# Performance work log

Hardware: AMD Instinct MI355X
Metric: run time of the kernel (lower is better)

Reference implementation:

```python
import jax, jax.numpy as jnp
import numpy as np

C, L, B = 66, 100, 4096
FEAT = 9 * C * 12  # 7128


def _conv1d(x, w, b, pad):
    # x: (B, Cin, L), w: (Cout, Cin, K), b: (Cout,)
    y = jax.lax.conv_general_dilated(x, w, (1,), [(pad, pad)],
                                     dimension_numbers=('NCH', 'OIH', 'NCH'))
    return y + b[None, :, None]


def _pool2(x):
    # AvgPool1d(kernel=2, stride=2) with floor on odd lengths
    Lx = x.shape[-1]
    x = x[..., : 2 * (Lx // 2)]
    return x.reshape(*x.shape[:-1], Lx // 2, 2).mean(-1)


def _branch(xc, w1, b1, w2, b2, w3, b3, pad):
    # conv/relu/pool x3 (dropout is identity in eval)
    h = _pool2(jax.nn.relu(_conv1d(xc, w1, b1, pad)))
    h = _pool2(jax.nn.relu(_conv1d(h, w2, b2, pad)))
    h = _pool2(jax.nn.relu(_conv1d(h, w3, b3, pad)))
    return h  # (B, 4, 12)


def setup_inputs() -> dict:
    key = jax.random.key(0)
    ks = jax.random.split(key, 20)
    s = 0.1
    inp = {
        'x': jax.random.normal(ks[0], (B, L, C), dtype=jnp.float32),
        # high-resolution branch (kernel 7, pad 3), one filter set per channel
        'hw1': jax.random.normal(ks[1], (C, 8, 1, 7)) * s,
        'hb1': jnp.full((C, 8), 0.1, jnp.float32),
        'hw2': jax.random.normal(ks[2], (C, 4, 8, 7)) * s,
        'hb2': jnp.full((C, 4), 0.1, jnp.float32),
        'hw3': jax.random.normal(ks[3], (C, 4, 4, 7)) * s,
        'hb3': jnp.full((C, 4), 0.1, jnp.float32),
        # low-resolution branch (kernel 3, pad 1)
        'lw1': jax.random.normal(ks[4], (C, 8, 1, 3)) * s,
        'lb1': jnp.full((C, 8), 0.1, jnp.float32),
        'lw2': jax.random.normal(ks[5], (C, 4, 8, 3)) * s,
        'lb2': jnp.full((C, 4), 0.1, jnp.float32),
        'lw3': jax.random.normal(ks[6], (C, 4, 4, 3)) * s,
        'lb3': jnp.full((C, 4), 0.1, jnp.float32),
        # MLP head
        'fw1': jax.random.normal(ks[7], (1936, FEAT)) * 0.02,
        'fb1': jnp.full((1936,), 0.1, jnp.float32),
        'fw2': jax.random.normal(ks[8], (14, 1936)) * 0.02,
        'fb2': jnp.full((14,), 0.1, jnp.float32),
    }
    return inp


def reference(x, hw1, hb1, hw2, hb2, hw3, hb3,
              lw1, lb1, lw2, lb2, lw3, lb3, fw1, fb1, fw2, fb2):
    bsz = x.shape[0]
    xc = jnp.transpose(x, (2, 0, 1))[:, :, None, :]  # (C, B, 1, L)
    high = jax.vmap(lambda xi, a, b_, c, d, e, f: _branch(xi, a, b_, c, d, e, f, 3))(
        xc, hw1, hb1, hw2, hb2, hw3, hb3)        # (C, B, 4, 12)
    low = jax.vmap(lambda xi, a, b_, c, d, e, f: _branch(xi, a, b_, c, d, e, f, 1))(
        xc, lw1, lb1, lw2, lb2, lw3, lb3)        # (C, B, 4, 12)
    res = jax.vmap(lambda xi: _pool2(_pool2(_pool2(xi))))(xc)  # (C, B, 1, 12)
    feats = jnp.concatenate([high, low, res], axis=2)          # (C, B, 9, 12)
    feats = jnp.transpose(feats, (1, 0, 2, 3)).reshape(bsz, -1)  # (B, C*9*12)
    h = jax.nn.relu(feats @ fw1.T + fb1)
    return h @ fw2.T + fb2
```

## Files before the change

kernel.cpp:

```cpp
#include <hip/hip_runtime.h>

typedef _Float16 f16;
typedef _Float16 h2 __attribute__((ext_vector_type(2)));
typedef _Float16 f16x8 __attribute__((ext_vector_type(8)));
typedef float    f32x4 __attribute__((ext_vector_type(4)));
typedef unsigned int u32;
typedef u32 u32x2 __attribute__((ext_vector_type(2)));
typedef u32 u32x4 __attribute__((ext_vector_type(4)));

#define CCH 66
#define LLEN 100
#define BSZ 4096
#define NPAD 2048
#define NOUT 1936
#define KFEAT 7128
#define FPC 112
#define KF2 (CCH * FPC)
#define KP2 7424
#define NCH2 (KP2 / 8)
#define ROWE (BSZ * 8)
#define LC (LLEN * CCH)
#define OSTR 25
#define XPW 52
#define CWS 512

typedef __attribute__((address_space(1))) const u32 gu32;
typedef __attribute__((address_space(3))) u32 lu32;

__device__ __forceinline__ void gload_lds16(const void* g, void* l) {
    __builtin_amdgcn_global_load_lds((gu32*)g, (lu32*)l, 16, 0, 0);
}

__device__ __forceinline__ h2  uh(u32 v) { return __builtin_bit_cast(h2, v); }
__device__ __forceinline__ u32 hu(h2 v)  { return __builtin_bit_cast(u32, v); }
__device__ __forceinline__ h2  pkfma(h2 a, h2 b, h2 c) { return __builtin_elementwise_fma(a, b, c); }
__device__ __forceinline__ h2  pkmax0(h2 a) { h2 z = (h2)(_Float16)0.f; return __builtin_elementwise_max(a, z); }

__global__ __launch_bounds__(256) void xpose_pack(const float* __restrict__ x,
                                                  u32* __restrict__ xP) {
    __shared__ float tile[64][133];
    const int w = blockIdx.x;
    const int b0 = blockIdx.y * 64;
    const int tid = threadIdx.x;
    const float* src = x + (size_t)b0 * LC + (size_t)(2 * w) * CCH;
#pragma unroll
    for (int i = 0; i < 33; ++i) {
        int f = i * 256 + tid;
        int bi = f / 132, j = f - bi * 132;
        tile[bi][j] = src[(size_t)bi * LC + j];
    }
    __syncthreads();
    const int lane = tid & 63, cg = tid >> 6;
    for (int c = cg; c < CCH; c += 4) {
        u32 v = hu((h2){(_Float16)tile[lane][c], (_Float16)tile[lane][66 + c]});
        xP[((size_t)c * XPW + w) * BSZ + b0 + lane] = v;
    }
}

__global__ __launch_bounds__(256) void zero_halo_xp(u32* __restrict__ xP) {
    const int c = blockIdx.x;
    const int i = blockIdx.y * 256 + threadIdx.x;
    *(u32x4*)(xP + ((size_t)c * XPW + 50) * BSZ + (size_t)i * 4) = (u32x4){0u, 0u, 0u, 0u};
}

__device__ __forceinline__ u32 dupf(float v) {
    _Float16 h = (_Float16)v; return hu((h2){h, h});
}
__device__ __forceinline__ u32 pk2f(float a, float b) {
    return hu((h2){(_Float16)a, (_Float16)b});
}

__global__ __launch_bounds__(64) void prep_w(
    const float* __restrict__ hw1, const float* __restrict__ hb1,
    const float* __restrict__ hw2, const float* __restrict__ hb2,
    const float* __restrict__ hw3, const float* __restrict__ hb3,
    const float* __restrict__ lw1, const float* __restrict__ lb1,
    const float* __restrict__ lw2, const float* __restrict__ lb2,
    const float* __restrict__ lw3, const float* __restrict__ lb3,
    u32* __restrict__ wpk) {
    const int c = blockIdx.x, t = threadIdx.x;
    u32* wb = wpk + c * CWS;
    for (int i = t; i < 56; i += 64) wb[i] = dupf(hw1[c * 56 + i]);
    if (t < 8)  wb[56 + t] = dupf(hb1[c * 8 + t]);
    for (int i = t; i < 224; i += 64) wb[64 + i] = dupf(hw2[c * 224 + i]);
    if (t < 4)  wb[288 + t] = dupf(hb2[c * 4 + t]);
    for (int i = t; i < 56; i += 64) {
        int pr = i / 28, j = i - pr * 28;
        wb[292 + i] = pk2f(hw3[c * 112 + 2 * pr * 28 + j], hw3[c * 112 + (2 * pr + 1) * 28 + j]);
    }
    if (t < 2)  wb[348 + t] = pk2f(hb3[c * 4 + 2 * t], hb3[c * 4 + 2 * t + 1]);
    for (int i = t; i < 24; i += 64) wb[350 + i] = dupf(lw1[c * 24 + i]);
    if (t < 8)  wb[374 + t] = dupf(lb1[c * 8 + t]);
    for (int i = t; i < 96; i += 64) wb[382 + i] = dupf(lw2[c * 96 + i]);
    if (t < 4)  wb[478 + t] = dupf(lb2[c * 4 + t]);
    for (int i = t; i < 24; i += 64) {
        int pr = i / 12, j = i - pr * 12;
        wb[482 + i] = pk2f(lw3[c * 48 + 2 * pr * 12 + j], lw3[c * 48 + (2 * pr + 1) * 12 + j]);
    }
    if (t < 2)  wb[506 + t] = pk2f(lb3[c * 4 + 2 * t], lb3[c * 4 + 2 * t + 1]);
}

template<int K>
__device__ __forceinline__ void hp1_core(const u32* PX, const u32* __restrict__ w1d,
                                         const u32* __restrict__ b1d, u32 msk, u32 np[8]) {
#pragma unroll
    for (int ic = 0; ic < 8; ++ic) {
        h2 bb = uh(b1d[ic]);
        h2 AL = bb, AH = bb;
#pragma unroll
        for (int k = 0; k < K; ++k) {
            h2 w = uh(w1d[ic * K + k]);
            AL = pkfma(w, uh(PX[k]), AL);
            AH = pkfma(w, uh(PX[k + 2]), AH);
        }
        AL = pkmax0(AL); AH = pkmax0(AH);
        _Float16 cA = (_Float16)0.5f * (AL.x + AL.y);
        _Float16 cB = (_Float16)0.5f * (AH.x + AH.y);
        np[ic] = hu((h2){cA, cB}) & msk;
    }
}

template<int K, int NA>
__device__ __forceinline__ void hp1_win(const u32 A[NA], int idx,
                                        const u32* w1d, const u32* b1d, u32 np[8]) {
    u32 PX[K + 2];
#pragma unroll
    for (int j = 0; j < K + 2; ++j)
        PX[j] = (j & 1) ? A[(j + 1) / 2]
                        : __builtin_amdgcn_alignbit(A[j / 2 + 1], A[j / 2], 16);
    u32 m = ((idx < 50) ? 0xFFFFu : 0u) | ((idx + 1 < 50) ? 0xFFFF0000u : 0u);
    hp1_core<K>(PX, w1d, b1d, m, np);
}

template<int K, int IDX>
__device__ __forceinline__ void hp1_edge(const u32* __restrict__ xg,
                                         const u32* w1d, const u32* b1d, u32 np[8]) {
    constexpr int P = K / 2;
    u32 PX[K + 2];
#pragma unroll
    for (int j = 0; j < K + 2; ++j) {
        int u = 2 * IDX - P + j;
        u32 v;
        if (u < -1)      v = 0u;
        else if (u == -1) v = xg[0] << 16;
        else if (u & 1)  v = __builtin_amdgcn_alignbit(xg[(size_t)((u + 1) / 2) * BSZ],
                                                       xg[(size_t)((u - 1) / 2) * BSZ], 16);
        else             v = xg[(size_t)(u / 2) * BSZ];
        PX[j] = v;
    }
    hp1_core<K>(PX, w1d, b1d, 0xFFFFFFFFu, np);
}

template<int K>
__device__ __forceinline__ void run_branch_pk(const u32* __restrict__ xg,
                                              const u32* __restrict__ wb,
                                              u32* __restrict__ orow) {
    constexpr int P = K / 2;
    constexpr int NW1 = (K + 1) / 2;
    constexpr int NA = (K == 7) ? 6 : 4;
    constexpr int WB = (K == 7) ? 3 : 2;
    const u32* w1d = wb;
    const u32* b1d = wb + 8 * K;
    const u32* w2d = b1d + 8;
    const u32* b2d = w2d + 32 * K;
    const u32* w3p = b2d + 4;
    const u32* b3p = w3p + 8 * K;

    u32 W1p[8][NW1];
    u32 W2d[4][K];
#pragma unroll
    for (int ic = 0; ic < 8; ++ic)
#pragma unroll
        for (int j = 0; j < NW1; ++j) W1p[ic][j] = 0u;
#pragma unroll
    for (int oc = 0; oc < 4; ++oc)
#pragma unroll
        for (int k = 0; k < K; ++k) W2d[oc][k] = 0u;

    {
        u32 np[8];
        if (K == 7) {
            hp1_edge<K, 0>(xg, w1d, b1d, np);
#pragma unroll
            for (int ic = 0; ic < 8; ++ic) W1p[ic][1] = np[ic] << 16;
            hp1_edge<K, 1>(xg, w1d, b1d, np);
#pragma unroll
            for (int ic = 0; ic < 8; ++ic) W1p[ic][2] = np[ic];
            hp1_edge<K, 3>(xg, w1d, b1d, np);
#pragma unroll
            for (int ic = 0; ic < 8; ++ic) W1p[ic][3] = np[ic];
        } else {
            hp1_edge<K, 0>(xg, w1d, b1d, np);
#pragma unroll
            for (int ic = 0; ic < 8; ++ic) W1p[ic][0] = np[ic] << 16;
            hp1_edge<K, 1>(xg, w1d, b1d, np);
#pragma unroll
            for (int ic = 0; ic < 8; ++ic) W1p[ic][1] = np[ic];
        }
    }

    u32 XA[NA];
#pragma unroll
    for (int j = 0; j < NA; ++j) XA[j] = xg[(size_t)(WB + j) * BSZ];

    h2 Pp01 = (h2)(_Float16)0.f, Pp23 = Pp01, Q01 = Pp01, Q23 = Pp01;
    const int SMAX = 23 + P;
    for (int s = 0; s <= SMAX; ++s) {
        h2 Y[4];
#pragma unroll
        for (int oc = 0; oc < 4; ++oc) Y[oc] = uh(b2d[oc]);
#pragma unroll
        for (int ic = 0; ic < 8; ++ic) {
            u32 PW[K];
#pragma unroll
            for (int k = 0; k < K; ++k)
                PW[k] = (k & 1) ? __builtin_amdgcn_alignbit(W1p[ic][k / 2 + 1], W1p[ic][k / 2], 16)
                                : W1p[ic][k / 2];
#pragma unroll
            for (int oc = 0; oc < 4; ++oc)
#pragma unroll
                for (int k = 0; k < K; ++k)
                    Y[oc] = pkfma(uh(w2d[(oc * 8 + ic) * K + k]), uh(PW[k]), Y[oc]);
        }
#pragma unroll
        for (int oc = 0; oc < 4; ++oc) {
            h2 Yr = pkmax0(Y[oc]);
            _Float16 hv = (_Float16)0.5f * (Yr.x + Yr.y);
            u32 d = hu((h2){hv, hv});
            d = (s <= 24) ? d : 0u;
#pragma unroll
            for (int k = 0; k < K - 1; ++k) W2d[oc][k] = W2d[oc][k + 1];
            W2d[oc][K - 1] = d;
        }
        int p = s - P;
        if (p >= 0) {
            h2 Y01 = uh(b3p[0]), Y23 = uh(b3p[1]);
#pragma unroll
            for (int ic = 0; ic < 4; ++ic)
#pragma unroll
                for (int k = 0; k < K; ++k) {
                    h2 wv = uh(W2d[ic][k]);
                    Y01 = pkfma(uh(w3p[ic * K + k]), wv, Y01);
                    Y23 = pkfma(uh(w3p[4 * K + ic * K + k]), wv, Y23);
                }
            Y01 = pkmax0(Y01); Y23 = pkmax0(Y23);
            if ((p & 1) == 0) { Pp01 = Y01; Pp23 = Y23; }
            else {
                h2 hf = (h2)(_Float16)0.5f;
                h2 O01 = (Pp01 + Y01) * hf;
                h2 O23 = (Pp23 + Y23) * hf;
                int t = p >> 1;
                if ((t & 1) == 0) { Q01 = O01; Q23 = O23; }
                else {
                    int w = t >> 1;
                    orow[0 * 6 + w] = hu((h2){Q01.x, O01.x});
                    orow[1 * 6 + w] = hu((h2){Q01.y, O01.y});
                    orow[2 * 6 + w] = hu((h2){Q23.x, O23.x});
                    orow[3 * 6 + w] = hu((h2){Q23.y, O23.y});
                }
            }
        }
        if (s < SMAX) {
            u32 np[8];
            hp1_win<K, NA>(XA, 2 * s + P + 2, w1d, b1d, np);
#pragma unroll
            for (int ic = 0; ic < 8; ++ic) {
#pragma unroll
                for (int j = 0; j < NW1 - 1; ++j) W1p[ic][j] = W1p[ic][j + 1];
                W1p[ic][NW1 - 1] = np[ic];
            }
#pragma unroll
            for (int j = 0; j < NA - 2; ++j) XA[j] = XA[j + 2];
            XA[NA - 2] = xg[(size_t)(WB + 2 * s + NA) * BSZ];
            XA[NA - 1] = xg[(size_t)(WB + 2 * s + NA + 1) * BSZ];
        }
    }
}

__global__ __launch_bounds__(256, 2) void feats_kernel(
    const u32* __restrict__ xP, const u32* __restrict__ wpk,
    f16* __restrict__ feats2) {
    __shared__ u32 obufw[256 * OSTR];
    const int c = blockIdx.x;
    const int tid = threadIdx.x;
    const int b = blockIdx.y * 256 + tid;

    const u32* xg = xP + (size_t)c * XPW * BSZ + b;
    const u32* wb = wpk + c * CWS;
    u32* orow = obufw + tid * OSTR;
    u32* dst = (u32*)feats2 + (size_t)c * 14 * (ROWE / 2) + (size_t)b * 4;

    run_branch_pk<7>(xg, wb, orow);
    {
        u32 v[24];
#pragma unroll
        for (int j = 0; j < 24; ++j) v[j] = orow[j];
#pragma unroll
        for (int ch = 0; ch < 6; ++ch)
            *(u32x4*)(dst + (size_t)ch * (ROWE / 2)) =
                (u32x4){v[ch * 4], v[ch * 4 + 1], v[ch * 4 + 2], v[ch * 4 + 3]};
    }
    run_branch_pk<3>(xg, wb + 350, orow);
    {
        u32 v[24];
#pragma unroll
        for (int j = 0; j < 24; ++j) v[j] = orow[j];
#pragma unroll
        for (int ch = 0; ch < 6; ++ch)
            *(u32x4*)(dst + (size_t)(6 + ch) * (ROWE / 2)) =
                (u32x4){v[ch * 4], v[ch * 4 + 1], v[ch * 4 + 2], v[ch * 4 + 3]};
    }
    u32 orr[6];
#pragma unroll
    for (int t2 = 0; t2 < 6; ++t2) {
        h2 S0 = uh(xg[(size_t)(8 * t2 + 0) * BSZ]) + uh(xg[(size_t)(8 * t2 + 1) * BSZ]) +
                uh(xg[(size_t)(8 * t2 + 2) * BSZ]) + uh(xg[(size_t)(8 * t2 + 3) * BSZ]);
        h2 S1 = uh(xg[(size_t)(8 * t2 + 4) * BSZ]) + uh(xg[(size_t)(8 * t2 + 5) * BSZ]) +
                uh(xg[(size_t)(8 * t2 + 6) * BSZ]) + uh(xg[(size_t)(8 * t2 + 7) * BSZ]);
        _Float16 o0 = (_Float16)0.125f * (S0.x + S0.y);
        _Float16 o1 = (_Float16)0.125f * (S1.x + S1.y);
        orr[t2] = hu((h2){o0, o1});
    }
    *(u32x4*)(dst + (size_t)12 * (ROWE / 2)) = (u32x4){orr[0], orr[1], orr[2], orr[3]};
    *(u32x4*)(dst + (size_t)13 * (ROWE / 2)) = (u32x4){orr[4], orr[5], 0u, 0u};
}

__global__ void zero_pad2(f16* __restrict__ feats2) {
    int idx = blockIdx.x * 256 + threadIdx.x;
    u32* dst = (u32*)(feats2 + (size_t)(CCH * 14) * ROWE);
    if (idx < (4 * ROWE * 2) / 16)
        *(u32x4*)(dst + idx * 4) = (u32x4){0u, 0u, 0u, 0u};
}

__global__ void cvt_fw1(const float* __restrict__ fw1, f16* __restrict__ dst) {
    int n = blockIdx.y;
    int kp = blockIdx.x * 256 + threadIdx.x;
    if (kp >= KP2) return;
    int c2 = kp / FPC, f = kp - c2 * FPC;
    float v = 0.f;
    if (n < NOUT && kp < KF2 && f < 108)
        v = fw1[(size_t)n * KFEAT + c2 * 108 + f];
    dst[(size_t)n * KP2 + kp] = (f16)v;
}

__global__ __launch_bounds__(256) void fc1_gemm(
    const f16* __restrict__ A, const f16* __restrict__ Bw, float* __restrict__ C) {
    __shared__ f16 lds_a[128 * 32];
    __shared__ f16 lds_b[128 * 32];
    const int tid = threadIdx.x;
    const int bm = blockIdx.x, bn = blockIdx.y, kz = blockIdx.z;
    const int wid = tid >> 6, lane = tid & 63;
    const int wm = wid >> 1, wn = wid & 1;

    f32x4 acc[4][4];
#pragma unroll
    for (int i = 0; i < 4; ++i)
#pragma unroll
        for (int j = 0; j < 4; ++j) acc[i][j] = (f32x4){0.f, 0.f, 0.f, 0.f};

    const f16* Bbase = Bw + (size_t)bn * 128 * KP2;
    const int l15 = lane & 15, lhi = lane >> 4;

    const int flat0 = tid, flat1 = 256 + tid;
    const int row0 = flat0 >> 2, kc0 = flat0 & 3;
    const int row1 = flat1 >> 2, kc1 = flat1 & 3;

    const int kbeg = kz * (KP2 / 2), kend = kbeg + KP2 / 2;
    for (int k0 = kbeg; k0 < kend; k0 += 32) {
        __syncthreads();
        gload_lds16(A + (size_t)((k0 >> 3) + kc0) * ROWE + (size_t)(bm * 128 + row0) * 8,
                    (char*)lds_a + flat0 * 16);
        gload_lds16(A + (size_t)((k0 >> 3) + kc1) * ROWE + (size_t)(bm * 128 + row1) * 8,
                    (char*)lds_a + flat1 * 16);
        gload_lds16(Bbase + (size_t)row0 * KP2 + k0 + kc0 * 8, (char*)lds_b + flat0 * 16);
        gload_lds16(Bbase + (size_t)row1 * KP2 + k0 + kc1 * 8, (char*)lds_b + flat1 * 16);
        __syncthreads();

        f16x8 af[4], bf[4];
#pragma unroll
        for (int i = 0; i < 4; ++i) {
            int m = wm * 64 + i * 16 + l15;
            af[i] = *(const f16x8*)(lds_a + m * 32 + lhi * 8);
            int n = wn * 64 + i * 16 + l15;
            bf[i] = *(const f16x8*)(lds_b + n * 32 + lhi * 8);
        }
#pragma unroll
        for (int i = 0; i < 4; ++i)
#pragma unroll
            for (int j = 0; j < 4; ++j)
                acc[i][j] = __builtin_amdgcn_mfma_f32_16x16x32_f16(af[i], bf[j], acc[i][j], 0, 0, 0);
    }

#pragma unroll
    for (int i = 0; i < 4; ++i)
#pragma unroll
        for (int j = 0; j < 4; ++j) {
            int n = bn * 128 + wn * 64 + j * 16 + l15;
#pragma unroll
            for (int r = 0; r < 4; ++r) {
                int m = bm * 128 + wm * 64 + i * 16 + lhi * 4 + r;
                atomicAdd(&C[(size_t)m * NPAD + n], acc[i][j][r]);
            }
        }
}

__global__ __launch_bounds__(256) void fc1_fin(const float* __restrict__ C,
                                               const float* __restrict__ fb1,
                                               f16* __restrict__ H) {
    size_t i4 = ((size_t)blockIdx.x * 256 + threadIdx.x) * 4;
    int n = (int)(i4 & (NPAD - 1));
    f32x4 v = *(const f32x4*)(C + i4);
    f16 r[4];
#pragma unroll
    for (int j = 0; j < 4; ++j) {
        int nn = n + j;
        float bias = (nn < NOUT) ? fb1[nn] : 0.f;
        r[j] = (f16)fmaxf(v[j] + bias, 0.f);
    }
    *(u32x2*)(H + i4) = (u32x2){hu((h2){r[0], r[1]}), hu((h2){r[2], r[3]})};
}

__global__ __launch_bounds__(64) void fc2_kernel(const f16* __restrict__ H,
                                                 const float* __restrict__ fw2,
                                                 const float* __restrict__ fb2,
                                                 float* __restrict__ out) {
    const int b = blockIdx.x;
    const int t = threadIdx.x;
    const f16* hb = H + (size_t)b * NPAD;
    float acc[14];
#pragma unroll
    for (int o = 0; o < 14; ++o) acc[o] = 0.f;
    for (int k = t; k < NOUT; k += 64) {
        float hv = (float)hb[k];
#pragma unroll
        for (int o = 0; o < 14; ++o) acc[o] += hv * fw2[o * NOUT + k];
    }
#pragma unroll
    for (int o = 0; o < 14; ++o) {
        float v = acc[o];
#pragma unroll
        for (int off = 32; off > 0; off >>= 1) v += __shfl_down(v, off, 64);
        if (t == 0) out[b * 14 + o] = v + fb2[o];
    }
}

extern "C" void kernel_launch(void* const* d_in, const int* in_sizes, int n_in,
                              void* d_out, int out_size, void* d_ws, size_t ws_size,
                              hipStream_t stream) {
    const float* x   = (const float*)d_in[0];
    const float* hw1 = (const float*)d_in[1];
    const float* hb1 = (const float*)d_in[2];
    const float* hw2 = (const float*)d_in[3];
    const float* hb2 = (const float*)d_in[4];
    const float* hw3 = (const float*)d_in[5];
    const float* hb3 = (const float*)d_in[6];
    const float* lw1 = (const float*)d_in[7];
    const float* lb1 = (const float*)d_in[8];
    const float* lw2 = (const float*)d_in[9];
    const float* lb2 = (const float*)d_in[10];
    const float* lw3 = (const float*)d_in[11];
    const float* lb3 = (const float*)d_in[12];
    const float* fw1 = (const float*)d_in[13];
    const float* fb1 = (const float*)d_in[14];
    const float* fw2 = (const float*)d_in[15];
    const float* fb2 = (const float*)d_in[16];

    char* wsb = (char*)d_ws;
    f16*  feats2 = (f16*)wsb;
    char* reg2   = wsb + (size_t)NCH2 * ROWE * 2;
    float* C     = (float*)reg2;
    f16*  h      = (f16*)(reg2 + (size_t)BSZ * NPAD * 4);
    char* reg3   = reg2 + 54067200;
    u32*  xP     = (u32*)reg3;
    f16*  fw1H   = (f16*)reg3;
    u32*  wpk    = (u32*)(reg3 + (size_t)CCH * XPW * BSZ * 4);

    xpose_pack<<<dim3(50, BSZ / 64), 256, 0, stream>>>(x, xP);
    zero_halo_xp<<<dim3(CCH, 8), 256, 0, stream>>>(xP);
    prep_w<<<dim3(CCH), 64, 0, stream>>>(hw1, hb1, hw2, hb2, hw3, hb3,
                                         lw1, lb1, lw2, lb2, lw3, lb3, wpk);
    feats_kernel<<<dim3(CCH, BSZ / 256), 256, 0, stream>>>(xP, wpk, feats2);
    zero_pad2<<<dim3(64), 256, 0, stream>>>(feats2);
    cvt_fw1<<<dim3((KP2 + 255) / 256, NPAD), 256, 0, stream>>>(fw1, fw1H);
    hipMemsetAsync(C, 0, (size_t)BSZ * NPAD * 4, stream);
    fc1_gemm<<<dim3(BSZ / 128, NPAD / 128, 2), 256, 0, stream>>>(feats2, fw1H, C);
    fc1_fin<<<dim3(BSZ * NPAD / 4 / 256), 256, 0, stream>>>(C, fb1, h);
    fc2_kernel<<<dim3(BSZ), 64, 0, stream>>>(h, fw2, fb2, (float*)d_out);
}
```

Measured before the change: 757.1 us.

## Drop split-K atomics in FC1 GEMM, fuse bias+ReLU epilogue, split feature branches

The FC1 GEMM no longer splits K across two blocks with fp32 atomicAdd into a zeroed buffer. Each block now runs the full K loop and writes the fp16 H output directly with bias and ReLU applied, which removes the memset, the atomics, the separate finalize kernel and a 32 MB fp32 intermediate. The feature kernel also gains a z dimension of 2, so the high- and low-resolution branches run in separate blocks for more parallelism. In exchange the GEMM grid is halved to 512 blocks, which may underfill the GPU, and the output stores are scalar fp16 writes.

After: 692.9 us. 1.09x faster.

```diff
diff --git a/kernel.cpp b/kernel.cpp
--- a/kernel.cpp
+++ b/kernel.cpp
@@ -290,8 +290,8 @@
     u32* orow = obufw + tid * OSTR;
     u32* dst = (u32*)feats2 + (size_t)c * 14 * (ROWE / 2) + (size_t)b * 4;
 
-    run_branch_pk<7>(xg, wb, orow);
-    {
+    if (blockIdx.z == 0) {
+        run_branch_pk<7>(xg, wb, orow);
         u32 v[24];
 #pragma unroll
         for (int j = 0; j < 24; ++j) v[j] = orow[j];
@@ -299,9 +299,8 @@
         for (int ch = 0; ch < 6; ++ch)
             *(u32x4*)(dst + (size_t)ch * (ROWE / 2)) =
                 (u32x4){v[ch * 4], v[ch * 4 + 1], v[ch * 4 + 2], v[ch * 4 + 3]};
-    }
-    run_branch_pk<3>(xg, wb + 350, orow);
-    {
+    } else {
+        run_branch_pk<3>(xg, wb + 350, orow);
         u32 v[24];
 #pragma unroll
         for (int j = 0; j < 24; ++j) v[j] = orow[j];
@@ -309,20 +308,20 @@
         for (int ch = 0; ch < 6; ++ch)
             *(u32x4*)(dst + (size_t)(6 + ch) * (ROWE / 2)) =
                 (u32x4){v[ch * 4], v[ch * 4 + 1], v[ch * 4 + 2], v[ch * 4 + 3]};
-    }
-    u32 orr[6];
-#pragma unroll
-    for (int t2 = 0; t2 < 6; ++t2) {
-        h2 S0 = uh(xg[(size_t)(8 * t2 + 0) * BSZ]) + uh(xg[(size_t)(8 * t2 + 1) * BSZ]) +
-                uh(xg[(size_t)(8 * t2 + 2) * BSZ]) + uh(xg[(size_t)(8 * t2 + 3) * BSZ]);
-        h2 S1 = uh(xg[(size_t)(8 * t2 + 4) * BSZ]) + uh(xg[(size_t)(8 * t2 + 5) * BSZ]) +
-                uh(xg[(size_t)(8 * t2 + 6) * BSZ]) + uh(xg[(size_t)(8 * t2 + 7) * BSZ]);
-        _Float16 o0 = (_Float16)0.125f * (S0.x + S0.y);
-        _Float16 o1 = (_Float16)0.125f * (S1.x + S1.y);
-        orr[t2] = hu((h2){o0, o1});
-    }
-    *(u32x4*)(dst + (size_t)12 * (ROWE / 2)) = (u32x4){orr[0], orr[1], orr[2], orr[3]};
-    *(u32x4*)(dst + (size_t)13 * (ROWE / 2)) = (u32x4){orr[4], orr[5], 0u, 0u};
+        u32 orr[6];
+#pragma unroll
+        for (int t2 = 0; t2 < 6; ++t2) {
+            h2 S0 = uh(xg[(size_t)(8 * t2 + 0) * BSZ]) + uh(xg[(size_t)(8 * t2 + 1) * BSZ]) +
+                    uh(xg[(size_t)(8 * t2 + 2) * BSZ]) + uh(xg[(size_t)(8 * t2 + 3) * BSZ]);
+            h2 S1 = uh(xg[(size_t)(8 * t2 + 4) * BSZ]) + uh(xg[(size_t)(8 * t2 + 5) * BSZ]) +
+                    uh(xg[(size_t)(8 * t2 + 6) * BSZ]) + uh(xg[(size_t)(8 * t2 + 7) * BSZ]);
+            _Float16 o0 = (_Float16)0.125f * (S0.x + S0.y);
+            _Float16 o1 = (_Float16)0.125f * (S1.x + S1.y);
+            orr[t2] = hu((h2){o0, o1});
+        }
+        *(u32x4*)(dst + (size_t)12 * (ROWE / 2)) = (u32x4){orr[0], orr[1], orr[2], orr[3]};
+        *(u32x4*)(dst + (size_t)13 * (ROWE / 2)) = (u32x4){orr[4], orr[5], 0u, 0u};
+    }
 }
 
 __global__ void zero_pad2(f16* __restrict__ feats2) {
@@ -344,11 +343,13 @@
 }
 
 __global__ __launch_bounds__(256) void fc1_gemm(
-    const f16* __restrict__ A, const f16* __restrict__ Bw, float* __restrict__ C) {
+    const f16* __restrict__ A, const f16* __restrict__ Bw,
+    const float* __restrict__ fb1, f16* __restrict__ H) {
     __shared__ f16 lds_a[128 * 32];
     __shared__ f16 lds_b[128 * 32];
     const int tid = threadIdx.x;
-    const int bm = blockIdx.x, bn = blockIdx.y, kz = blockIdx.z;
+    const int bm = blockIdx.x;
+    const int bn = blockIdx.y;
     const int wid = tid >> 6, lane = tid & 63;
     const int wm = wid >> 1, wn = wid & 1;
 
@@ -365,8 +366,7 @@
     const int row0 = flat0 >> 2, kc0 = flat0 & 3;
     const int row1 = flat1 >> 2, kc1 = flat1 & 3;
 
-    const int kbeg = kz * (KP2 / 2), kend = kbeg + KP2 / 2;
-    for (int k0 = kbeg; k0 < kend; k0 += 32) {
+    for (int k0 = 0; k0 < KP2; k0 += 32) {
         __syncthreads();
         gload_lds16(A + (size_t)((k0 >> 3) + kc0) * ROWE + (size_t)(bm * 128 + row0) * 8,
                     (char*)lds_a + flat0 * 16);
@@ -392,32 +392,19 @@
     }
 
 #pragma unroll
-    for (int i = 0; i < 4; ++i)
+    for (int i = 0; i < 4; ++i) {
 #pragma unroll
         for (int j = 0; j < 4; ++j) {
             int n = bn * 128 + wn * 64 + j * 16 + l15;
+            float bias = (n < NOUT) ? fb1[n] : 0.f;
 #pragma unroll
             for (int r = 0; r < 4; ++r) {
                 int m = bm * 128 + wm * 64 + i * 16 + lhi * 4 + r;
-                atomicAdd(&C[(size_t)m * NPAD + n], acc[i][j][r]);
+                float v = acc[i][j][r] + bias;
+                H[(size_t)m * NPAD + n] = (f16)fmaxf(v, 0.f);
             }
         }
-}
-
-__global__ __launch_bounds__(256) void fc1_fin(const float* __restrict__ C,
-                                               const float* __restrict__ fb1,
-                                               f16* __restrict__ H) {
-    size_t i4 = ((size_t)blockIdx.x * 256 + threadIdx.x) * 4;
-    int n = (int)(i4 & (NPAD - 1));
-    f32x4 v = *(const f32x4*)(C + i4);
-    f16 r[4];
-#pragma unroll
-    for (int j = 0; j < 4; ++j) {
-        int nn = n + j;
-        float bias = (nn < NOUT) ? fb1[nn] : 0.f;
-        r[j] = (f16)fmaxf(v[j] + bias, 0.f);
-    }
-    *(u32x2*)(H + i4) = (u32x2){hu((h2){r[0], r[1]}), hu((h2){r[2], r[3]})};
+    }
 }
 
 __global__ __launch_bounds__(64) void fc2_kernel(const f16* __restrict__ H,
@@ -468,8 +455,7 @@
     char* wsb = (char*)d_ws;
     f16*  feats2 = (f16*)wsb;
     char* reg2   = wsb + (size_t)NCH2 * ROWE * 2;
-    float* C     = (float*)reg2;
-    f16*  h      = (f16*)(reg2 + (size_t)BSZ * NPAD * 4);
+    f16*  h      = (f16*)reg2;
     char* reg3   = reg2 + 54067200;
     u32*  xP     = (u32*)reg3;
     f16*  fw1H   = (f16*)reg3;
@@ -479,11 +465,9 @@
     zero_halo_xp<<<dim3(CCH, 8), 256, 0, stream>>>(xP);
     prep_w<<<dim3(CCH), 64, 0, stream>>>(hw1, hb1, hw2, hb2, hw3, hb3,
                                          lw1, lb1, lw2, lb2, lw3, lb3, wpk);
-    feats_kernel<<<dim3(CCH, BSZ / 256), 256, 0, stream>>>(xP, wpk, feats2);
+    feats_kernel<<<dim3(CCH, BSZ / 256, 2), 256, 0, stream>>>(xP, wpk, feats2);
     zero_pad2<<<dim3(64), 256, 0, stream>>>(feats2);
     cvt_fw1<<<dim3((KP2 + 255) / 256, NPAD), 256, 0, stream>>>(fw1, fw1H);
-    hipMemsetAsync(C, 0, (size_t)BSZ * NPAD * 4, stream);
-    fc1_gemm<<<dim3(BSZ / 128, NPAD / 128, 2), 256, 0, stream>>>(feats2, fw1H, C);
-    fc1_fin<<<dim3(BSZ * NPAD / 4 / 256), 256, 0, stream>>>(C, fb1, h);
+    fc1_gemm<<<dim3(BSZ / 128, NPAD / 128), 256, 0, stream>>>(feats2, fw1H, fb1, h);
     fc2_kernel<<<dim3(BSZ), 64, 0, stream>>>(h, fw2, fb2, (float*)d_out);
 }
```
